# Performance work log

Measured on AMD Instinct MI355X. Metric: run time of the kernel, lower is better.

The kernel has to match this reference:

```python
import jax, jax.numpy as jnp
import numpy as np

K, NC, NA = 9, 13, 5
NB, NH, NW = 128, 26, 26
NT, L = 50, 2 * K + 3
NOOBJ, OBJ, SIL = 1.0, 5.0, 0.6
COORD_S, CLASS_S = 1.0, 1.0
PRETRAIN_EPOCHS = 15
TH, SHARP = 80.0, 2.0                      # corner-conf distance threshold (px), sharpness
SCALE = np.array([640.0, 480.0], np.float32)  # im_width, im_height used by corner_confidences
CONF0 = float(np.exp(SHARP) - 1.0)
ANCHORS = np.array([1.482, 2.2412, 2.0501, 3.1265, 2.3946, 4.6891,
                    3.1018, 3.991, 3.4879, 5.8851], np.float32).reshape(NA, 2)


def setup_inputs():
    k1, k2 = jax.random.split(jax.random.key(0))
    output = jax.random.normal(k1, (NB, NA * (2 * K + 1 + NC), NH, NW), dtype=jnp.float32)
    target = jax.random.uniform(k2, (NB, NT * L), dtype=jnp.float32)
    return {"output": output, "target": target, "epoch": 20}


def _corner_conf(pred, gt):
    # pred, gt: [..., K, 2] normalized corners -> mean per-corner confidence [...]
    d = jnp.sqrt((((pred - gt) * jnp.asarray(SCALE)) ** 2).sum(-1))  # pixel distance [..., K]
    c = (jnp.exp(SHARP * (1.0 - d / TH)) - 1.0) / CONF0
    return jnp.where(d < TH, c, 0.0).mean(-1)


def _region_loss(output, target, epoch):
    nAnch, nPix = NA * NH * NW, NH * NW
    tgt = jax.lax.stop_gradient(target).reshape(NB, NT, L)
    out = output.reshape(NB, NA, 2 * K + 1 + NC, NH, NW)
    # keypoint 0 gets sigmoid, the rest are raw offsets
    xs = jnp.concatenate([jax.nn.sigmoid(out[:, :, 0:1]), out[:, :, 2:2 * K:2]], axis=2)  # [B,A,K,H,W]
    ys = jnp.concatenate([jax.nn.sigmoid(out[:, :, 1:2]), out[:, :, 3:2 * K:2]], axis=2)
    conf = jax.nn.sigmoid(out[:, :, 2 * K])                             # [B,A,H,W]
    cls_logits = jnp.transpose(out[:, :, 2 * K + 1:], (0, 1, 3, 4, 2))  # [B,A,H,W,NC]

    gxg = jnp.arange(NW, dtype=jnp.float32)
    gyg = jnp.arange(NH, dtype=jnp.float32)
    px = (jax.lax.stop_gradient(xs) + gxg) / NW            # detached, as torch uses .data
    py = (jax.lax.stop_gradient(ys) + gyg[:, None]) / NH
    # pred corners per anchor cell, flat anchor index = a*H*W + j*W + i -> [B, A*H*W, K, 2]
    pc = jnp.transpose(jnp.stack([px, py], -1), (0, 1, 3, 4, 2, 5)).reshape(NB, nAnch, K, 2)

    gt_xy = tgt[:, :, 1:1 + 2 * K].reshape(NB, NT, K, 2)
    # torch loop breaks at first target with x1 == 0 -> cumulative validity
    valid = jnp.cumprod((tgt[:, :, 1] != 0).astype(jnp.int32), axis=1) > 0  # [B,T]

    # pass 1: max corner confidence over valid GT, per anchor cell
    def max_conf_step(cur, inp):
        gt_t, v_t = inp                                    # [B,K,2], [B]
        c = _corner_conf(pc, gt_t[:, None]).reshape(NB, NA, NH, NW)
        return jnp.where(v_t[:, None, None, None], jnp.maximum(cur, c), cur), None

    cur_confs, _ = jax.lax.scan(max_conf_step, jnp.zeros((NB, NA, NH, NW), jnp.float32),
                                (jnp.swapaxes(gt_xy, 0, 1), valid.T))
    conf_mask0 = jnp.where(cur_confs > SIL, 0.0, NOOBJ)

    # per-target quantities (vectorized over b,t)
    gx = gt_xy[..., 0] * NW                                # [B,T,K]
    gy = gt_xy[..., 1] * NH
    gi0 = jnp.clip(jnp.floor(gx[:, :, 0]).astype(jnp.int32), 0, NW - 1)  # [B,T]
    gj0 = jnp.clip(jnp.floor(gy[:, :, 0]).astype(jnp.int32), 0, NH - 1)
    # pred_box is fetched with best_n == -1 (as in the source); emulate torch negative flat index via mod
    flat_idx = jnp.mod(jnp.arange(NB)[:, None] * nAnch - nPix + gj0 * NW + gi0, NB * nAnch)
    pred_box = pc.reshape(NB * nAnch, K, 2)[flat_idx]      # [B,T,K,2]
    conf_t = _corner_conf(pred_box, gt_xy)                 # [B,T]
    gw = tgt[:, :, L - 2] * NW
    gh = tgt[:, :, L - 1] * NH
    aw, ah = ANCHORS[:, 0], ANCHORS[:, 1]
    mw = jnp.minimum(aw, gw[..., None])                    # centered-box IoU (bbox_iou, cxcywh)
    mh = jnp.minimum(ah, gh[..., None])
    inter = mw * mh
    iou = inter / (aw * ah + (gw * gh)[..., None] - inter)
    best_n = jnp.argmax(iou, axis=-1).astype(jnp.int32)    # [B,T] (first max, like strict '>')
    txv = gx - gi0[..., None].astype(jnp.float32)          # [B,T,K]
    tyv = gy - gj0[..., None].astype(jnp.float32)
    tclsv = tgt[:, :, 0]

    # pass 2: sequential scatter matching torch overwrite order over t
    barange = jnp.arange(NB)
    z = jnp.zeros((NB, NA, NH, NW), jnp.float32)
    zk = jnp.zeros((NB, NA, NH, NW, K), jnp.float32)

    def scatter_step(carry, inp):
        cm, clm, cfm, tx, ty, tcf, tcl = carry
        v, bn, gj, gi, cft, txt, tyt, tct = inp
        idx = (barange, bn, gj, gi)
        vk = v[:, None]
        cm = cm.at[idx].set(jnp.where(v, 1.0, cm[idx]))
        clm = clm.at[idx].set(jnp.where(v, 1.0, clm[idx]))
        cfm = cfm.at[idx].set(jnp.where(v, OBJ, cfm[idx]))
        tx = tx.at[idx].set(jnp.where(vk, txt, tx[idx]))
        ty = ty.at[idx].set(jnp.where(vk, tyt, ty[idx]))
        tcf = tcf.at[idx].set(jnp.where(v, cft, tcf[idx]))
        tcl = tcl.at[idx].set(jnp.where(v, tct, tcl[idx]))
        return (cm, clm, cfm, tx, ty, tcf, tcl), None

    inps = (valid.T, best_n.T, gj0.T, gi0.T, conf_t.T,
            jnp.swapaxes(txv, 0, 1), jnp.swapaxes(tyv, 0, 1), tclsv.T)
    (coord_mask, cls_mask, conf_mask, tx, ty, tconf, tcls), _ = jax.lax.scan(
        scatter_step, (z, z, conf_mask0, zk, zk, z, z), inps)

    # losses
    xsT = jnp.transpose(xs, (0, 1, 3, 4, 2))               # [B,A,H,W,K]
    ysT = jnp.transpose(ys, (0, 1, 3, 4, 2))
    cmk = coord_mask[..., None]
    loss_x = 0.5 * COORD_S * jnp.sum(((xsT - tx) * cmk) ** 2)
    loss_y = 0.5 * COORD_S * jnp.sum(((ysT - ty) * cmk) ** 2)
    sq = jnp.sqrt(conf_mask)
    loss_conf = 0.5 * jnp.sum(((conf - tconf) * sq) ** 2)
    labels = jnp.clip(tcls.astype(jnp.int32), 0, NC - 1)
    ce = -jnp.take_along_axis(jax.nn.log_softmax(cls_logits, axis=-1),
                              labels[..., None], axis=-1)[..., 0]
    loss_cls = CLASS_S * jnp.sum(ce * cls_mask)
    loss = loss_x + loss_y + loss_cls
    if epoch > PRETRAIN_EPOCHS:
        loss = loss + loss_conf
    return loss


def reference(output, target, epoch):
    return _region_loss(output, target, epoch)
```

## Files before the change

### kernel.cpp

```cpp
#include <hip/hip_runtime.h>
#include <math.h>
#include <stdint.h>

#define KK     9
#define NCLS   13
#define NANC   5
#define NBB    128
#define NHH    26
#define NWW    26
#define NTT    50
#define LL     21
#define CHC    32
#define NPIX   676
#define NANCHT 3380
#define NCELLT 432640
#define GTS    20
#define MWPB   106
#define GTH_W  12
#define NBLKX  53
#define QMAX   3200

#define LOG2E_F   1.4426950408889634f
#define K1C       2.8853900817779268f
#define K2C       0.036067376022224085f
#define SXW       24.615384615384617f
#define SYH       18.461538461538463f
#define THRESH_S  43.500902934225507f
#define CONF_T_SCALE 0.017390849194407297f
#define OBJ_W     5.0f
#define EPOCH_PRETRAIN 15
#define BIGV      6.0e18f

#define CULL_H2   0.36f
#define HSCALE    0.03125f

typedef __attribute__((ext_vector_type(2))) float f2;
typedef __attribute__((ext_vector_type(2))) _Float16 h2;
typedef __attribute__((ext_vector_type(4))) unsigned int u4;
typedef __attribute__((ext_vector_type(2))) unsigned int u2;

static __device__ __forceinline__ float fast_exp2(float x){
  return __builtin_amdgcn_exp2f(x);
}
static __device__ __forceinline__ float fast_sqrt(float x){
  return __builtin_amdgcn_sqrtf(x);
}
static __device__ __forceinline__ float sigmoidf_(float x){
  return 1.0f/(1.0f + fast_exp2(-LOG2E_F*x));
}
static __device__ __forceinline__ h2 cvt_pkrtz_(float a, float b){
  return __builtin_bit_cast(h2, __builtin_amdgcn_cvt_pkrtz(a, b));
}

__constant__ float c_anch[10] = {1.482f,2.2412f,2.0501f,3.1265f,2.3946f,4.6891f,
                                 3.1018f,3.991f,3.4879f,5.8851f};


__global__ __launch_bounds__(64) void prep_kernel(const float* __restrict__ tgt,
                                                  float* __restrict__ gts_neg,
                                                  unsigned int* __restrict__ gth,
                                                  int* __restrict__ nvalid){
  int b = blockIdx.x;
  int t = threadIdx.x;
  const float* trow = tgt + (size_t)b*NTT*LL;
  float v1 = (t < NTT) ? trow[t*LL + 1] : 0.0f;
  unsigned long long mk = __ballot(t < NTT && v1 != 0.0f);
  int firstInvalid = __ffsll(~mk) - 1;
  if (t == 0) nvalid[b] = firstInvalid;
  for (int idx = t; idx < NTT*GTS; idx += 64){
    int tt = idx / GTS;
    int c  = idx - tt*GTS;
    float v;
    if (c == 9 || c == 19)      v = BIGV;
    else if (c < 9)             v = -(trow[tt*LL + 1 + 2*c] * 640.0f);
    else                        v = -(trow[tt*LL + 2 + 2*(c-10)] * 480.0f);
    gts_neg[(size_t)b*NTT*GTS + idx] = v;
  }
  for (int idx = t; idx < NTT*GTH_W; idx += 64){
    int tt = idx / GTH_W;
    int w  = idx - tt*GTH_W;
    const float* tr2 = trow + tt*LL;
    float a0 = BIGV, a1 = BIGV;
    if (w < 5){
      int k0 = 2*w;
      a0 = -(tr2[1 + 2*k0] * 20.0f);
      if (k0 + 1 < KK) a1 = -(tr2[1 + 2*(k0+1)] * 20.0f);
    } else if (w < 10){
      int k0 = 2*(w-5);
      a0 = -(tr2[2 + 2*k0] * 15.0f);
      if (k0 + 1 < KK) a1 = -(tr2[2 + 2*(k0+1)] * 15.0f);
    }
    h2 hh; hh.x = (_Float16)a0; hh.y = (_Float16)a1;
    gth[(size_t)b*NTT*GTH_W + idx] = __builtin_bit_cast(unsigned int, hh);
  }
}

__global__ __launch_bounds__(256) void region_confmask_kernel(
    const float* __restrict__ outp, const float* __restrict__ gts_neg,
    const unsigned int* __restrict__ gth,
    const int* __restrict__ nvalid, unsigned int* __restrict__ maskw,
    double* __restrict__ partials){
  int b    = blockIdx.y;
  int tid  = threadIdx.x;
  int lane = tid & 63;
  int w    = tid >> 6;
  int cellbase = blockIdx.x * 64;
  int cell = cellbase + lane;
  bool live = (cell < NANCHT);
  int cellc = live ? cell : (NANCHT-1);

  __shared__ float sgt[NTT*GTS] __attribute__((aligned(16)));
  __shared__ unsigned int sgh[NTT*GTH_W] __attribute__((aligned(16)));
  __shared__ f2 sPx[5*64] __attribute__((aligned(8)));
  __shared__ f2 sPy[5*64] __attribute__((aligned(8)));
  __shared__ float sCf[64];
  __shared__ unsigned short qlist[QMAX];
  __shared__ int qcount;
  __shared__ unsigned int sexclw[2];

  if (tid == 0) qcount = 0;
  if (tid < 2) sexclw[tid] = 0u;

  {
    const float* fsrc = gts_neg + (size_t)b*NTT*GTS;
    for (int idx = tid; idx < NTT*GTS; idx += 256) sgt[idx] = fsrc[idx];
    const unsigned int* gsrc = gth + (size_t)b*NTT*GTH_W;
    for (int idx = tid; idx < NTT*GTH_W; idx += 256) sgh[idx] = gsrc[idx];
  }

  {
    int a   = cellc / NPIX;
    int rem = cellc - a*NPIX;
    int jj  = rem / NWW;
    int ii  = rem - jj*NWW;
    const float* cb = outp + (((size_t)b*NANC + a)*CHC)*NPIX + rem;
    for (int ch = w; ch <= 18; ch += 4){
      float raw = cb[(size_t)ch * NPIX];
      if (ch == 18){
        sCf[lane] = sigmoidf_(raw);
      } else {
        int k = ch >> 1, axis = ch & 1;
        float r = (k == 0) ? sigmoidf_(raw) : raw;
        float v = axis ? (r + (float)jj) * SYH : (r + (float)ii) * SXW;
        float* dst = axis ? (float*)sPy : (float*)sPx;
        dst[(((k >> 1)*64) + lane)*2 + (k & 1)] = v;
      }
    }
  }
  __syncthreads();

  h2 Pxh[5], Pyh[5];
#pragma unroll
  for (int p = 0; p < 5; ++p){
    f2 px = sPx[p*64 + lane];
    f2 py = sPy[p*64 + lane];
    if (p == 4){ px.y = 0.0f; py.y = 0.0f; }
    px *= HSCALE; py *= HSCALE;
    Pxh[p] = cvt_pkrtz_(px.x, px.y);
    Pyh[p] = cvt_pkrtz_(py.x, py.y);
  }

  int nv = nvalid[b];
  int t0 = (w*nv) >> 2;
  int t1 = ((w+1)*nv) >> 2;
  const _Float16 thh = (_Float16)CULL_H2;
#pragma unroll 2
  for (int t = t0; t < t1; ++t){
    const u4* q = (const u4*)(sgh + t*GTH_W);
    u4 q0 = q[0];
    u4 q1 = q[1];
    u2 q2 = *(const u2*)(sgh + t*GTH_W + 8);
    h2 Xa[5] = { __builtin_bit_cast(h2, q0.x), __builtin_bit_cast(h2, q0.y),
                 __builtin_bit_cast(h2, q0.z), __builtin_bit_cast(h2, q0.w),
                 __builtin_bit_cast(h2, q1.x) };
    h2 Ya[5] = { __builtin_bit_cast(h2, q1.y), __builtin_bit_cast(h2, q1.z),
                 __builtin_bit_cast(h2, q1.w), __builtin_bit_cast(h2, q2.x),
                 __builtin_bit_cast(h2, q2.y) };
    h2 m2 = {(_Float16)60000.0f, (_Float16)60000.0f};
#pragma unroll
    for (int p = 0; p < 5; ++p){
      h2 dx = Pxh[p] + Xa[p];
      h2 dy = Pyh[p] + Ya[p];
      h2 r  = __builtin_elementwise_fma(dy, dy, dx*dx);
      m2 = __builtin_elementwise_min(m2, r);
    }
    _Float16 mm = (m2.x < m2.y) ? m2.x : m2.y;
    if (mm < thh){
      int qi = atomicAdd(&qcount, 1);
      qlist[qi] = (unsigned short)(lane | (t << 6));
    }
  }
  __syncthreads();

  int n = qcount;
  for (int idx = tid; idx < n; idx += 256){
    unsigned int pkid = qlist[idx];
    int l2 = pkid & 63;
    int t  = pkid >> 6;
    const float* gg = sgt + t*GTS;
    float s = 0.0f;
#pragma unroll
    for (int p = 0; p < 5; ++p){
      f2 px = sPx[p*64 + l2];
      f2 py = sPy[p*64 + l2];
      {
        float dx = px.x + gg[2*p];
        float dy = py.x + gg[10 + 2*p];
        float d  = fast_sqrt(fmaf(dy, dy, dx*dx));
        float e  = fast_exp2(fmaf(d, -K2C, K1C));
        s += fmaxf(e, 1.0f);
      }
      if (p < 4){
        float dx = px.y + gg[2*p + 1];
        float dy = py.y + gg[10 + 2*p + 1];
        float d  = fast_sqrt(fmaf(dy, dy, dx*dx));
        float e  = fast_exp2(fmaf(d, -K2C, K1C));
        s += fmaxf(e, 1.0f);
      }
    }
    if (s > THRESH_S) atomicOr(&sexclw[l2 >> 5], 1u << (l2 & 31));
  }
  __syncthreads();

  if (w == 0){
    unsigned int ex = sexclw[lane >> 5];
    int m0 = ((ex >> (lane & 31)) & 1u) ? 0 : 1;
    float cf = sCf[lane];
    float contrib = (m0 && live) ? 0.5f*cf*cf : 0.0f;

    unsigned long long mb = __ballot(m0 != 0);
    if ((lane & 31) == 0){
      unsigned int wv = (lane == 0) ? (unsigned int)mb : (unsigned int)(mb >> 32);
      maskw[(size_t)b*MWPB + (cellbase >> 5) + (lane >> 5)] = wv;
    }

#pragma unroll
    for (int o = 32; o > 0; o >>= 1) contrib += __shfl_xor(contrib, o, 64);
    if (lane == 0)
      partials[(size_t)b*NBLKX + blockIdx.x] = (double)contrib;
  }
}

__global__ __launch_bounds__(64) void scatter_loss_kernel(
    const float* __restrict__ outp, const float* __restrict__ tgt,
    const int* __restrict__ nvalid, const unsigned int* __restrict__ maskw,
    double* __restrict__ bc_part){
  int b = blockIdx.x;
  int t = threadIdx.x;
  __shared__ int keys[NTT];
  int nv = nvalid[b];
  bool valid = (t < nv);

  int key = -1, gi0 = 0, gj0 = 0, bn = 0;
  float txv[KK], tyv[KK];
  float conf_t = 0.0f, tcls = 0.0f;

  if (t < NTT){
    const float* trow = tgt + ((size_t)b*NTT + t)*LL;
    tcls = trow[0];
    float gx0 = trow[1]*(float)NWW;
    float gy0 = trow[2]*(float)NHH;
    gi0 = min(max((int)floorf(gx0), 0), NWW-1);
    gj0 = min(max((int)floorf(gy0), 0), NHH-1);
#pragma unroll
    for (int k = 0; k < KK; ++k){
      txv[k] = trow[1+2*k]*(float)NWW - (float)gi0;
      tyv[k] = trow[2+2*k]*(float)NHH - (float)gj0;
    }
    float gw = trow[LL-2]*(float)NWW, gh = trow[LL-1]*(float)NHH;
    float best = -1.0f;
    for (int a = 0; a < NANC; ++a){
      float aw = c_anch[2*a], ah = c_anch[2*a+1];
      float inter = fminf(aw, gw) * fminf(ah, gh);
      float iou = inter / (aw*ah + gw*gh - inter);
      if (iou > best){ best = iou; bn = a; }
    }
    key = bn*NPIX + gj0*NWW + gi0;
    keys[t] = key;

    long f = (long)b*NANCHT - NPIX + gj0*NWW + gi0;
    if (f < 0) f += NCELLT;
    int bb  = (int)(f / NANCHT);
    int rr  = (int)(f - (long)bb*NANCHT);
    int aa  = rr / NPIX;
    int rr2 = rr - aa*NPIX;
    int jj  = rr2 / NWW;
    int ii  = rr2 - jj*NWW;
    const float* pbase = outp + (((size_t)bb*NANC + aa)*CHC)*NPIX + rr2;
    float s = 0.0f;
#pragma unroll
    for (int k = 0; k < KK; ++k){
      float rx = pbase[(2*k)*NPIX], ry = pbase[(2*k+1)*NPIX];
      if (k == 0){ rx = sigmoidf_(rx); ry = sigmoidf_(ry); }
      float Pxx = (rx + (float)ii)*SXW, Pyy = (ry + (float)jj)*SYH;
      float dx = Pxx - trow[1+2*k]*640.0f;
      float dy = Pyy - trow[2+2*k]*480.0f;
      float d  = fast_sqrt(fmaf(dy, dy, dx*dx));
      float e  = fast_exp2(fmaf(d, -K2C, K1C));
      s += fmaxf(e, 1.0f);
    }
    conf_t = (s - 9.0f) * CONF_T_SCALE;
  }
  __syncthreads();

  bool winner = valid;
  if (valid){
    for (int u = t+1; u < nv; ++u) if (keys[u] == key){ winner = false; break; }
  }

  double lx = 0.0, ly = 0.0, lcls = 0.0, lcf = 0.0;
  if (winner){
    const float* cbase = outp + (((size_t)b*NANC + bn)*CHC)*NPIX + gj0*NWW + gi0;
    float sx = 0.0f, sy = 0.0f;
#pragma unroll
    for (int k = 0; k < KK; ++k){
      float rx = cbase[(2*k)*NPIX], ry = cbase[(2*k+1)*NPIX];
      if (k == 0){ rx = sigmoidf_(rx); ry = sigmoidf_(ry); }
      float dx = rx - txv[k], dy = ry - tyv[k];
      sx = fmaf(dx, dx, sx); sy = fmaf(dy, dy, sy);
    }
    lx = 0.5*(double)sx; ly = 0.5*(double)sy;

    float lg[NCLS], mx = -1e30f;
#pragma unroll
    for (int c = 0; c < NCLS; ++c){ lg[c] = cbase[(2*KK+1+c)*NPIX]; mx = fmaxf(mx, lg[c]); }
    float se = 0.0f;
#pragma unroll
    for (int c = 0; c < NCLS; ++c) se += fast_exp2((lg[c]-mx)*LOG2E_F);
    int label = min(max((int)tcls, 0), NCLS-1);
    lcls = (double)(mx + logf(se) - lg[label]);

    float cf = sigmoidf_(cbase[(2*KK)*NPIX]);
    int idx = bn*NPIX + gj0*NWW + gi0;
    int m0 = (maskw[(size_t)b*MWPB + (idx >> 5)] >> (idx & 31)) & 1;
    float dcf = cf - conf_t;
    lcf = 0.5*OBJ_W*(double)(dcf*dcf) - (m0 ? 0.5*(double)(cf*cf) : 0.0);
  }

#pragma unroll
  for (int o = 32; o > 0; o >>= 1){
    lx  += __shfl_xor(lx,  o, 64);
    ly  += __shfl_xor(ly,  o, 64);
    lcls+= __shfl_xor(lcls,o, 64);
    lcf += __shfl_xor(lcf, o, 64);
  }
  if (threadIdx.x == 0){
    double* bp = bc_part + (size_t)b*4;
    bp[0] = lx; bp[1] = ly; bp[2] = lcls; bp[3] = lcf;
  }
}

__global__ __launch_bounds__(256) void finalize_kernel(
    const double* __restrict__ bc_part, const double* __restrict__ partials,
    const int* __restrict__ epoch_p, float* __restrict__ outv){
  int tid = threadIdx.x;
  double vx=0, vy=0, vc=0, vf=0, vb=0;
  for (int i = tid; i < NBB; i += 256){
    vx += bc_part[4*i]; vy += bc_part[4*i+1];
    vc += bc_part[4*i+2]; vf += bc_part[4*i+3];
  }
  for (int i = tid; i < NBLKX*NBB; i += 256) vb += partials[i];
#pragma unroll
  for (int o = 32; o > 0; o >>= 1){
    vx += __shfl_xor(vx, o, 64); vy += __shfl_xor(vy, o, 64);
    vc += __shfl_xor(vc, o, 64); vf += __shfl_xor(vf, o, 64);
    vb += __shfl_xor(vb, o, 64);
  }
  __shared__ double sm[5][4];
  int wid = tid >> 6, lane = tid & 63;
  if (lane == 0){ sm[0][wid]=vx; sm[1][wid]=vy; sm[2][wid]=vc; sm[3][wid]=vf; sm[4][wid]=vb; }
  __syncthreads();
  if (tid == 0){
    double fx=0, fy=0, fc=0, ff=0, fb=0;
    for (int w = 0; w < 4; ++w){ fx+=sm[0][w]; fy+=sm[1][w]; fc+=sm[2][w]; ff+=sm[3][w]; fb+=sm[4][w]; }
    double loss = fx + fy + fc;
    if (*epoch_p > EPOCH_PRETRAIN) loss += ff + fb;
    outv[0] = (float)loss;
  }
}

extern "C" void kernel_launch(void* const* d_in, const int* in_sizes, int n_in,
                              void* d_out, int out_size, void* d_ws, size_t ws_size,
                              hipStream_t stream){
  (void)in_sizes; (void)n_in; (void)out_size; (void)ws_size;
  const float* outp = (const float*)d_in[0];
  const float* tgt  = (const float*)d_in[1];
  const int*   ep   = (const int*)d_in[2];
  float* outv = (float*)d_out;
  char* ws = (char*)d_ws;

  double* bc_part  = (double*)(ws);
  double* partials = (double*)(ws + 4096);
  float*  gts_neg  = (float*) (ws + 58368);
  int*    nvalid   = (int*)   (ws + 570368);
  unsigned int* maskw = (unsigned int*)(ws + 570880);
  unsigned int* gth   = (unsigned int*)(ws + 625152);

  prep_kernel<<<dim3(NBB), dim3(64), 0, stream>>>(tgt, gts_neg, gth, nvalid);
  region_confmask_kernel<<<dim3(NBLKX, NBB), dim3(256), 0, stream>>>(outp, gts_neg, gth, nvalid, maskw, partials);
  scatter_loss_kernel<<<dim3(NBB), dim3(64), 0, stream>>>(outp, tgt, nvalid, maskw, bc_part);
  finalize_kernel<<<dim3(1), dim3(256), 0, stream>>>(bc_part, partials, ep, outv);
}
```

Baseline: 145.2 us.

## Replace brute-force fp16 target culling with spatial bin grid of target bitmasks

The prep kernel now bins each valid target's keypoints into a coarse per-keypoint 2D grid of 19.2px bins. Each bin's 3x3 neighbourhood gets an atomic OR with the target's bit into a 64-bit mask, and a per-row occupancy bitmap is kept alongside. The confmask kernel then looks up each predicted corner's bin to gather candidate targets directly, instead of testing every target with packed half-precision distance math. Candidates go into the queue through a wave-level prefix sum with one atomic per wave, replacing one LDS atomic per hit. The cost is a multi-megabyte workspace memset each call, global atomics in prep, and scattered global gathers per corner.

```diff
diff --git a/kernel.cpp b/kernel.cpp
--- a/kernel.cpp
+++ b/kernel.cpp
@@ -16,9 +16,14 @@
 #define NCELLT 432640
 #define GTS    20
 #define MWPB   106
-#define GTH_W  12
 #define NBLKX  53
 #define QMAX   3200
+
+#define BINNX  34
+#define BINNY  25
+#define BININV (1.0f/19.2f)
+#define BPB    (KK*BINNY)
+#define MPB    (KK*BINNY*BINNX)
 
 #define LOG2E_F   1.4426950408889634f
 #define K1C       2.8853900817779268f
@@ -31,13 +36,7 @@
 #define EPOCH_PRETRAIN 15
 #define BIGV      6.0e18f
 
-#define CULL_H2   0.36f
-#define HSCALE    0.03125f
-
 typedef __attribute__((ext_vector_type(2))) float f2;
-typedef __attribute__((ext_vector_type(2))) _Float16 h2;
-typedef __attribute__((ext_vector_type(4))) unsigned int u4;
-typedef __attribute__((ext_vector_type(2))) unsigned int u2;
 
 static __device__ __forceinline__ float fast_exp2(float x){
   return __builtin_amdgcn_exp2f(x);
@@ -48,26 +47,30 @@
 static __device__ __forceinline__ float sigmoidf_(float x){
   return 1.0f/(1.0f + fast_exp2(-LOG2E_F*x));
 }
-static __device__ __forceinline__ h2 cvt_pkrtz_(float a, float b){
-  return __builtin_bit_cast(h2, __builtin_amdgcn_cvt_pkrtz(a, b));
-}
 
 __constant__ float c_anch[10] = {1.482f,2.2412f,2.0501f,3.1265f,2.3946f,4.6891f,
                                  3.1018f,3.991f,3.4879f,5.8851f};
 
 
-__global__ __launch_bounds__(64) void prep_kernel(const float* __restrict__ tgt,
-                                                  float* __restrict__ gts_neg,
-                                                  unsigned int* __restrict__ gth,
-                                                  int* __restrict__ nvalid){
+__global__ __launch_bounds__(256) void prep_kernel(const float* __restrict__ tgt,
+                                                   float* __restrict__ gts_neg,
+                                                   unsigned long long* __restrict__ masksD,
+                                                   unsigned long long* __restrict__ bitmapD,
+                                                   int* __restrict__ nvalid){
   int b = blockIdx.x;
-  int t = threadIdx.x;
+  int tid = threadIdx.x;
   const float* trow = tgt + (size_t)b*NTT*LL;
-  float v1 = (t < NTT) ? trow[t*LL + 1] : 0.0f;
-  unsigned long long mk = __ballot(t < NTT && v1 != 0.0f);
-  int firstInvalid = __ffsll(~mk) - 1;
-  if (t == 0) nvalid[b] = firstInvalid;
-  for (int idx = t; idx < NTT*GTS; idx += 64){
+  __shared__ int snv;
+  if (tid < 64){
+    float v1 = (tid < NTT) ? trow[tid*LL + 1] : 0.0f;
+    unsigned long long mk = __ballot(tid < NTT && v1 != 0.0f);
+    int firstInvalid = __ffsll(~mk) - 1;
+    if (tid == 0){ snv = firstInvalid; nvalid[b] = firstInvalid; }
+  }
+  __syncthreads();
+  int nv = snv;
+
+  for (int idx = tid; idx < NTT*GTS; idx += 256){
     int tt = idx / GTS;
     int c  = idx - tt*GTS;
     float v;
@@ -76,28 +79,37 @@
     else                        v = -(trow[tt*LL + 2 + 2*(c-10)] * 480.0f);
     gts_neg[(size_t)b*NTT*GTS + idx] = v;
   }
-  for (int idx = t; idx < NTT*GTH_W; idx += 64){
-    int tt = idx / GTH_W;
-    int w  = idx - tt*GTH_W;
-    const float* tr2 = trow + tt*LL;
-    float a0 = BIGV, a1 = BIGV;
-    if (w < 5){
-      int k0 = 2*w;
-      a0 = -(tr2[1 + 2*k0] * 20.0f);
-      if (k0 + 1 < KK) a1 = -(tr2[1 + 2*(k0+1)] * 20.0f);
-    } else if (w < 10){
-      int k0 = 2*(w-5);
-      a0 = -(tr2[2 + 2*k0] * 15.0f);
-      if (k0 + 1 < KK) a1 = -(tr2[2 + 2*(k0+1)] * 15.0f);
-    }
-    h2 hh; hh.x = (_Float16)a0; hh.y = (_Float16)a1;
-    gth[(size_t)b*NTT*GTH_W + idx] = __builtin_bit_cast(unsigned int, hh);
+
+  unsigned long long* mb_ = masksD  + (size_t)b*MPB;
+  unsigned long long* bb_ = bitmapD + (size_t)b*BPB;
+  for (int idx = tid; idx < NTT*KK; idx += 256){
+    int t = idx / KK, k = idx - t*KK;
+    if (t >= nv) continue;
+    float gx = trow[t*LL + 1 + 2*k] * 640.0f;
+    float gy = trow[t*LL + 2 + 2*k] * 480.0f;
+    int bx = (int)floorf(gx * BININV);
+    int by = (int)floorf(gy * BININV);
+    bx = min(max(bx, 0), BINNX-1);
+    by = min(max(by, 0), BINNY-1);
+    unsigned long long tb = 1ull << t;
+    unsigned long long rowbits = (bx == 0) ? 3ull : (7ull << (bx-1));
+    for (int dy = -1; dy <= 1; ++dy){
+      int yy = by + dy;
+      if (yy < 0 || yy > BINNY-1) continue;
+      atomicOr(&bb_[k*BINNY + yy], rowbits);
+      for (int dx = -1; dx <= 1; ++dx){
+        int xx = bx + dx;
+        if (xx < 0 || xx > BINNX-1) continue;
+        atomicOr(&mb_[(k*BINNY + yy)*BINNX + xx], tb);
+      }
+    }
   }
 }
 
 __global__ __launch_bounds__(256) void region_confmask_kernel(
     const float* __restrict__ outp, const float* __restrict__ gts_neg,
-    const unsigned int* __restrict__ gth,
+    const unsigned long long* __restrict__ masksD,
+    const unsigned long long* __restrict__ bitmapD,
     const int* __restrict__ nvalid, unsigned int* __restrict__ maskw,
     double* __restrict__ partials){
   int b    = blockIdx.y;
@@ -110,7 +122,7 @@
   int cellc = live ? cell : (NANCHT-1);
 
   __shared__ float sgt[NTT*GTS] __attribute__((aligned(16)));
-  __shared__ unsigned int sgh[NTT*GTH_W] __attribute__((aligned(16)));
+  __shared__ unsigned long long sbm[BPB];
   __shared__ f2 sPx[5*64] __attribute__((aligned(8)));
   __shared__ f2 sPy[5*64] __attribute__((aligned(8)));
   __shared__ float sCf[64];
@@ -124,8 +136,8 @@
   {
     const float* fsrc = gts_neg + (size_t)b*NTT*GTS;
     for (int idx = tid; idx < NTT*GTS; idx += 256) sgt[idx] = fsrc[idx];
-    const unsigned int* gsrc = gth + (size_t)b*NTT*GTH_W;
-    for (int idx = tid; idx < NTT*GTH_W; idx += 256) sgh[idx] = gsrc[idx];
+    const unsigned long long* bsrc = bitmapD + (size_t)b*BPB;
+    if (tid < BPB) sbm[tid] = bsrc[tid];
   }
 
   {
@@ -149,45 +161,50 @@
   }
   __syncthreads();
 
-  h2 Pxh[5], Pyh[5];
+  const unsigned long long* mbase = masksD + (size_t)b*MPB;
+  int nv = nvalid[b];
+  unsigned long long vmask = (nv >= 64) ? ~0ull : ((1ull << nv) - 1ull);
+  unsigned long long qbits = 0ull;
 #pragma unroll
   for (int p = 0; p < 5; ++p){
     f2 px = sPx[p*64 + lane];
     f2 py = sPy[p*64 + lane];
-    if (p == 4){ px.y = 0.0f; py.y = 0.0f; }
-    px *= HSCALE; py *= HSCALE;
-    Pxh[p] = cvt_pkrtz_(px.x, px.y);
-    Pyh[p] = cvt_pkrtz_(py.x, py.y);
-  }
-
-  int nv = nvalid[b];
-  int t0 = (w*nv) >> 2;
-  int t1 = ((w+1)*nv) >> 2;
-  const _Float16 thh = (_Float16)CULL_H2;
-#pragma unroll 2
-  for (int t = t0; t < t1; ++t){
-    const u4* q = (const u4*)(sgh + t*GTH_W);
-    u4 q0 = q[0];
-    u4 q1 = q[1];
-    u2 q2 = *(const u2*)(sgh + t*GTH_W + 8);
-    h2 Xa[5] = { __builtin_bit_cast(h2, q0.x), __builtin_bit_cast(h2, q0.y),
-                 __builtin_bit_cast(h2, q0.z), __builtin_bit_cast(h2, q0.w),
-                 __builtin_bit_cast(h2, q1.x) };
-    h2 Ya[5] = { __builtin_bit_cast(h2, q1.y), __builtin_bit_cast(h2, q1.z),
-                 __builtin_bit_cast(h2, q1.w), __builtin_bit_cast(h2, q2.x),
-                 __builtin_bit_cast(h2, q2.y) };
-    h2 m2 = {(_Float16)60000.0f, (_Float16)60000.0f};
-#pragma unroll
-    for (int p = 0; p < 5; ++p){
-      h2 dx = Pxh[p] + Xa[p];
-      h2 dy = Pyh[p] + Ya[p];
-      h2 r  = __builtin_elementwise_fma(dy, dy, dx*dx);
-      m2 = __builtin_elementwise_min(m2, r);
-    }
-    _Float16 mm = (m2.x < m2.y) ? m2.x : m2.y;
-    if (mm < thh){
-      int qi = atomicAdd(&qcount, 1);
-      qlist[qi] = (unsigned short)(lane | (t << 6));
+    {
+      int k  = 2*p;
+      int bx = min(max((int)floorf(px.x * BININV), 0), BINNX-1);
+      int by = min(max((int)floorf(py.x * BININV), 0), BINNY-1);
+      if ((sbm[k*BINNY + by] >> bx) & 1ull)
+        qbits |= mbase[((size_t)(k*BINNY + by))*BINNX + bx];
+    }
+    if (p < 4){
+      int k  = 2*p + 1;
+      int bx = min(max((int)floorf(px.y * BININV), 0), BINNX-1);
+      int by = min(max((int)floorf(py.y * BININV), 0), BINNY-1);
+      if ((sbm[k*BINNY + by] >> bx) & 1ull)
+        qbits |= mbase[((size_t)(k*BINNY + by))*BINNX + bx];
+    }
+  }
+  qbits &= vmask;
+
+  {
+    int n = __popcll(qbits);
+    int pref = n;
+#pragma unroll
+    for (int o = 1; o < 64; o <<= 1){
+      int v = __shfl_up(pref, o, 64);
+      if (lane >= o) pref += v;
+    }
+    int tot  = __shfl(pref, 63, 64);
+    int excl = pref - n;
+    int wbase = 0;
+    if (lane == 63 && tot > 0) wbase = atomicAdd(&qcount, tot);
+    wbase = __shfl(wbase, 63, 64);
+    int slot = wbase + excl;
+    unsigned long long qb = qbits;
+    while (qb){
+      int t = __ffsll((long long)qb) - 1;
+      qb &= qb - 1;
+      qlist[slot++] = (unsigned short)(lane | (t << 6));
     }
   }
   __syncthreads();
@@ -394,10 +411,13 @@
   float*  gts_neg  = (float*) (ws + 58368);
   int*    nvalid   = (int*)   (ws + 570368);
   unsigned int* maskw = (unsigned int*)(ws + 570880);
-  unsigned int* gth   = (unsigned int*)(ws + 625152);
-
-  prep_kernel<<<dim3(NBB), dim3(64), 0, stream>>>(tgt, gts_neg, gth, nvalid);
-  region_confmask_kernel<<<dim3(NBLKX, NBB), dim3(256), 0, stream>>>(outp, gts_neg, gth, nvalid, maskw, partials);
+  unsigned long long* masksD  = (unsigned long long*)(ws + 625152);
+  unsigned long long* bitmapD = (unsigned long long*)(ws + 8458752);
+
+  hipMemsetAsync(ws + 625152, 0, (size_t)NBB*MPB*8 + (size_t)NBB*BPB*8, stream);
+
+  prep_kernel<<<dim3(NBB), dim3(256), 0, stream>>>(tgt, gts_neg, masksD, bitmapD, nvalid);
+  region_confmask_kernel<<<dim3(NBLKX, NBB), dim3(256), 0, stream>>>(outp, gts_neg, masksD, bitmapD, nvalid, maskw, partials);
   scatter_loss_kernel<<<dim3(NBB), dim3(64), 0, stream>>>(outp, tgt, nvalid, maskw, bc_part);
   finalize_kernel<<<dim3(1), dim3(256), 0, stream>>>(bc_part, partials, ep, outv);
 }
```

New measurement: 179.8 us. 23.9% more time.
